# Performance work log

Hardware: AMD Instinct MI355X
Metric: run time of the kernel (lower is better)

## Reference

```python
import jax, jax.numpy as jnp
import numpy as np

LN_EPS = 1e-5


def setup_inputs() -> dict:
    key = jax.random.key(0)
    ks = jax.random.split(key, 5)
    dim, hidden = 512, 8
    B, S = 128, 1024
    x = jax.random.normal(ks[0], (B, S, dim), dtype=jnp.float32)
    # torch Linear: weight [out, in], bias [out]
    w1 = jax.random.normal(ks[1], (hidden, dim), dtype=jnp.float32) * (1.0 / np.sqrt(dim))
    b1 = jax.random.normal(ks[2], (hidden,), dtype=jnp.float32) * 0.02
    w2 = jax.random.normal(ks[3], (dim, hidden), dtype=jnp.float32) * (1.0 / np.sqrt(hidden))
    b2 = jax.random.normal(ks[4], (dim,), dtype=jnp.float32) * 0.02
    gamma = jnp.ones((dim,), dtype=jnp.float32)
    beta = jnp.zeros((dim,), dtype=jnp.float32)
    return {"x": x, "w1": w1, "b1": b1, "w2": w2, "b2": b2,
            "gamma": gamma, "beta": beta}


def _layernorm(y, gamma, beta):
    mu = jnp.mean(y, axis=-1, keepdims=True)
    var = jnp.mean(jnp.square(y - mu), axis=-1, keepdims=True)
    return (y - mu) * jax.lax.rsqrt(var + LN_EPS) * gamma + beta


def reference(x, w1, b1, w2, b2, gamma, beta):
    # y = gelu(gelu(LN(x) @ W1^T + b1) @ W2^T + b2) + x  (exact erf GELU, as torch nn.GELU default)
    y = _layernorm(x, gamma, beta)                       # [B,S,D]
    h = jnp.einsum('bsd,hd->bsh', y, w1) + b1            # [B,S,8]
    h = jax.nn.gelu(h, approximate=False)
    o = jnp.einsum('bsh,dh->bsd', h, w2) + b2            # [B,S,D]
    o = jax.nn.gelu(o, approximate=False)
    return o + x
```

## Files before the change

### kernel.cpp

```cpp
#include <hip/hip_runtime.h>
#include <math.h>

#define DIM 512
#define HID 8
#define LN_EPS 1e-5f

typedef float  f32x4 __attribute__((ext_vector_type(4)));
typedef __fp16 h16x2 __attribute__((ext_vector_type(2)));

#define DPP_XOR1 0xB1
#define DPP_XOR2 0x4E
#define DPP_HM   0x141
#define DPP_ROR8 0x128
#define DPP_ROR4 0x124

template <int CTRL>
__device__ __forceinline__ float dpp_movf(float v) {
    int r = __builtin_amdgcn_update_dpp(0, __builtin_bit_cast(int, v),
                                        CTRL, 0xF, 0xF, true);
    return __builtin_bit_cast(float, r);
}
template <int CTRL>
__device__ __forceinline__ float dpp_addf(float v) {
    return v + dpp_movf<CTRL>(v);
}
__device__ __forceinline__ float readlanef(float v, int lane) {
    return __builtin_bit_cast(float,
        __builtin_amdgcn_readlane(__builtin_bit_cast(int, v), lane));
}

__device__ __forceinline__ float gelu_fast(float v) {
    const float C = 0.044715f;
    const float K = 2.30258819f;
    float v2 = v * v;
    float t  = v * fmaf(C, v2, 1.0f);
    float e  = __builtin_amdgcn_exp2f(K * t);
    float r  = __builtin_amdgcn_rcpf(e + 1.0f);
    return fmaf(-v, r, v);
}

__device__ __forceinline__ float wave_sum(float v) {
    v = dpp_addf<DPP_XOR1>(v);
    v = dpp_addf<DPP_XOR2>(v);
    v = dpp_addf<DPP_HM>(v);
    v = dpp_addf<DPP_ROR8>(v);
    return (readlanef(v, 0) + readlanef(v, 16))
         + (readlanef(v, 32) + readlanef(v, 48));
}

__device__ __forceinline__ float reduce8(float ph[8], int lj) {
#pragma unroll
    for (int j = 0; j < 8; ++j) ph[j] = dpp_addf<DPP_XOR1>(ph[j]);
#pragma unroll
    for (int j = 0; j < 8; ++j) ph[j] = dpp_addf<DPP_XOR2>(ph[j]);
#pragma unroll
    for (int j = 0; j < 8; ++j) ph[j] = dpp_addf<DPP_HM>(ph[j]);
    float sel = ph[0];
    sel = (lj == 1) ? ph[1] : sel;
    sel = (lj == 2) ? ph[2] : sel;
    sel = (lj == 3) ? ph[3] : sel;
    sel = (lj == 4) ? ph[4] : sel;
    sel = (lj == 5) ? ph[5] : sel;
    sel = (lj == 6) ? ph[6] : sel;
    sel = (lj == 7) ? ph[7] : sel;
    sel = dpp_addf<DPP_ROR8>(sel);
    sel += __shfl_xor(sel, 16, 64);
    sel += __shfl_xor(sel, 32, 64);
    return sel;
}

__device__ __forceinline__ void load8(float* dst, const float* __restrict__ src) {
    const f32x4* p = reinterpret_cast<const f32x4*>(src);
    f32x4 a = p[0];
    f32x4 b = p[1];
    dst[0] = a.x; dst[1] = a.y; dst[2] = a.z; dst[3] = a.w;
    dst[4] = b.x; dst[5] = b.y; dst[6] = b.z; dst[7] = b.w;
}

__global__ __launch_bounds__(256)
__attribute__((amdgpu_waves_per_eu(4)))
void mlp_fused_kernel(const float* __restrict__ x,
                      const float* __restrict__ w1,
                      const float* __restrict__ b1,
                      const float* __restrict__ w2,
                      const float* __restrict__ b2,
                      const float* __restrict__ gamma,
                      const float* __restrict__ beta,
                      float* __restrict__ out,
                      int nrows, int rows_per_wave) {
    const int lane  = threadIdx.x & 63;
    const int wav   = threadIdx.x >> 6;
    const int wgid  = blockIdx.x * 4 + wav;
    const int dbase = lane * 8;
    const int lj    = lane & 7;

    const int r0 = wgid * rows_per_wave;
    if (r0 >= nrows) return;
    int r1 = r0 + rows_per_wave;
    if (r1 > nrows) r1 = nrows;

    float gm[8], bt[8];
    load8(gm, gamma + dbase);
    load8(bt, beta  + dbase);

    h16x2 w1p[32];
    float w1sp[8], c1p[8];
#pragma unroll
    for (int j = 0; j < 8; ++j) { w1sp[j] = 0.f; c1p[j] = 0.f; }
#pragma unroll
    for (int j = 0; j < 8; ++j) {
        float raw[8];
        load8(raw, w1 + j * DIM + dbase);
#pragma unroll
        for (int k = 0; k < 8; ++k)
            c1p[j] = fmaf(bt[k], raw[k], c1p[j]);
#pragma unroll
        for (int i = 0; i < 4; ++i) {
            float a = raw[2 * i]     * gm[2 * i];
            float b = raw[2 * i + 1] * gm[2 * i + 1];
            h16x2 p = __builtin_amdgcn_cvt_pkrtz(a, b);
            w1p[j * 4 + i] = p;
            w1sp[j] += (float)p.x + (float)p.y;
        }
    }
    const float W1s = reduce8(w1sp, lj);
    const float b1e = b1[lj] + reduce8(c1p, lj);

    h16x2 w2pk[32];
#pragma unroll
    for (int k = 0; k < 8; ++k)
#pragma unroll
        for (int i = 0; i < 4; ++i) {
            float a = w2[(size_t)(dbase + k) * HID + (lj ^ (2 * i))];
            float b = w2[(size_t)(dbase + k) * HID + (lj ^ (2 * i + 1))];
            w2pk[k * 4 + i] = __builtin_amdgcn_cvt_pkrtz(a, b);
        }

    float b2r[8];
    load8(b2r, b2 + dbase);

    float xv[8];
    load8(xv, x + (size_t)r0 * DIM + dbase);

    for (int r = r0; r < r1; ++r) {
        float xn[8];
        const int rn = (r + 1 < r1) ? (r + 1) : r;
        load8(xn, x + (size_t)rn * DIM + dbase);

        float s = 0.f, q = 0.f;
#pragma unroll
        for (int k = 0; k < 8; ++k) { s += xv[k]; q = fmaf(xv[k], xv[k], q); }

        h16x2 xh[4];
#pragma unroll
        for (int i = 0; i < 4; ++i)
            xh[i] = __builtin_amdgcn_cvt_pkrtz(xv[2 * i], xv[2 * i + 1]);

        float ph[8];
#pragma unroll
        for (int j = 0; j < 8; ++j) {
            float a = 0.f;
#pragma unroll
            for (int i = 0; i < 4; ++i)
                a = __builtin_amdgcn_fdot2(xh[i], w1p[j * 4 + i], a, false);
            ph[j] = a;
        }

        const float sw = wave_sum(s);
        const float qw = wave_sum(q);
        const float Hw = reduce8(ph, lj);

        const float mu  = sw * (1.0f / DIM);
        const float var = qw * (1.0f / DIM) - mu * mu;
        const float rs  = rsqrtf(var + LN_EPS);

        const float h = gelu_fast(fmaf(rs, fmaf(-mu, W1s, Hw), b1e));

        float hj0 = h;
        float hj1 = dpp_movf<DPP_XOR1>(hj0);
        float hj2 = dpp_movf<DPP_XOR2>(hj0);
        float hj3 = dpp_movf<DPP_XOR2>(hj1);
        float hj4 = dpp_movf<DPP_ROR4>(hj0);
        float hj5 = dpp_movf<DPP_ROR4>(hj1);
        float hj6 = dpp_movf<DPP_ROR4>(hj2);
        float hj7 = dpp_movf<DPP_ROR4>(hj3);
        h16x2 hp[4];
        hp[0] = __builtin_amdgcn_cvt_pkrtz(hj0, hj1);
        hp[1] = __builtin_amdgcn_cvt_pkrtz(hj2, hj3);
        hp[2] = __builtin_amdgcn_cvt_pkrtz(hj4, hj5);
        hp[3] = __builtin_amdgcn_cvt_pkrtz(hj6, hj7);

        f32x4 o0, o1;
#pragma unroll
        for (int k = 0; k < 8; ++k) {
            float o = b2r[k];
#pragma unroll
            for (int i = 0; i < 4; ++i)
                o = __builtin_amdgcn_fdot2(hp[i], w2pk[k * 4 + i], o, false);
            float val = gelu_fast(o) + xv[k];
            if (k < 4) o0[k] = val; else o1[k - 4] = val;
        }

        float* po = out + (size_t)r * DIM + dbase;
        __builtin_nontemporal_store(o0, reinterpret_cast<f32x4*>(po));
        __builtin_nontemporal_store(o1, reinterpret_cast<f32x4*>(po) + 1);

#pragma unroll
        for (int k = 0; k < 8; ++k) xv[k] = xn[k];
    }
}

extern "C" void kernel_launch(void* const* d_in, const int* in_sizes, int n_in,
                              void* d_out, int out_size, void* d_ws, size_t ws_size,
                              hipStream_t stream) {
    const float* x     = (const float*)d_in[0];
    const float* w1    = (const float*)d_in[1];
    const float* b1    = (const float*)d_in[2];
    const float* w2    = (const float*)d_in[3];
    const float* b2    = (const float*)d_in[4];
    const float* gamma = (const float*)d_in[5];
    const float* beta  = (const float*)d_in[6];
    float* out = (float*)d_out;

    const int nrows  = in_sizes[0] / DIM;
    const int blocks = 1024;
    const int total_waves = blocks * 4;
    const int rows_per_wave = (nrows + total_waves - 1) / total_waves;

    mlp_fused_kernel<<<blocks, 256, 0, stream>>>(
        x, w1, b1, w2, b2, gamma, beta, out, nrows, rows_per_wave);
}
```

Measured before the change: 143.6 us.

## Stage packed fp16 weights in LDS and double the grid to raise occupancy

Each workgroup now converts W1 (pre-scaled by gamma) and W2 to packed fp16 once into shared memory, with an XOR swizzle on W2, instead of every lane holding 64 packed weight registers. The per-row matvecs read weight vectors back from LDS. The layer-1 activations are broadcast with readlane rather than a DPP permutation. The waves_per_eu hint is dropped and the grid goes from 1024 to 2048 blocks. The aim is lower VGPR pressure and more resident waves to better hide HBM latency on this bandwidth-bound kernel, at the cost of extra LDS reads on every row and a per-block weight setup.

Measured after the change: 168.4 us. +17.2%, slower.

```diff
diff --git a/kernel.cpp b/kernel.cpp
--- a/kernel.cpp
+++ b/kernel.cpp
@@ -7,12 +7,12 @@
 
 typedef float  f32x4 __attribute__((ext_vector_type(4)));
 typedef __fp16 h16x2 __attribute__((ext_vector_type(2)));
+typedef __fp16 h16x8 __attribute__((ext_vector_type(8)));
 
 #define DPP_XOR1 0xB1
 #define DPP_XOR2 0x4E
 #define DPP_HM   0x141
 #define DPP_ROR8 0x128
-#define DPP_ROR4 0x124
 
 template <int CTRL>
 __device__ __forceinline__ float dpp_movf(float v) {
@@ -78,7 +78,6 @@
 }
 
 __global__ __launch_bounds__(256)
-__attribute__((amdgpu_waves_per_eu(4)))
 void mlp_fused_kernel(const float* __restrict__ x,
                       const float* __restrict__ w1,
                       const float* __restrict__ b1,
@@ -88,57 +87,91 @@
                       const float* __restrict__ beta,
                       float* __restrict__ out,
                       int nrows, int rows_per_wave) {
-    const int lane  = threadIdx.x & 63;
-    const int wav   = threadIdx.x >> 6;
-    const int wgid  = blockIdx.x * 4 + wav;
+    __shared__ __fp16 w1h[8 * DIM];
+    __shared__ __fp16 w2h[DIM * HID];
+
+    const int tid  = threadIdx.x;
+    const int lane = tid & 63;
+    const int wav  = tid >> 6;
+    const int lj   = lane & 7;
     const int dbase = lane * 8;
-    const int lj    = lane & 7;
-
+
+    {
+        const int j  = tid >> 5;
+        const int d0 = (tid & 31) * 16;
+        const float* wsrc = w1 + j * DIM + d0;
+        const float* gsrc = gamma + d0;
+        h16x8 p0, p1;
+#pragma unroll
+        for (int i = 0; i < 4; ++i) {
+            float a = wsrc[2 * i]     * gsrc[2 * i];
+            float b = wsrc[2 * i + 1] * gsrc[2 * i + 1];
+            h16x2 p = __builtin_amdgcn_cvt_pkrtz(a, b);
+            p0[2 * i] = p.x; p0[2 * i + 1] = p.y;
+        }
+#pragma unroll
+        for (int i = 0; i < 4; ++i) {
+            float a = wsrc[8 + 2 * i]     * gsrc[8 + 2 * i];
+            float b = wsrc[8 + 2 * i + 1] * gsrc[8 + 2 * i + 1];
+            h16x2 p = __builtin_amdgcn_cvt_pkrtz(a, b);
+            p1[2 * i] = p.x; p1[2 * i + 1] = p.y;
+        }
+        *reinterpret_cast<h16x8*>(&w1h[j * DIM + d0])     = p0;
+        *reinterpret_cast<h16x8*>(&w1h[j * DIM + d0 + 8]) = p1;
+
+#pragma unroll
+        for (int rr = 0; rr < 2; ++rr) {
+            const int d = tid + rr * 256;
+            const float* src = w2 + (size_t)d * HID;
+            f32x4 a = *reinterpret_cast<const f32x4*>(src);
+            f32x4 b = *reinterpret_cast<const f32x4*>(src + 4);
+            h16x8 pk;
+            h16x2 q0 = __builtin_amdgcn_cvt_pkrtz(a.x, a.y);
+            h16x2 q1 = __builtin_amdgcn_cvt_pkrtz(a.z, a.w);
+            h16x2 q2 = __builtin_amdgcn_cvt_pkrtz(b.x, b.y);
+            h16x2 q3 = __builtin_amdgcn_cvt_pkrtz(b.z, b.w);
+            pk[0] = q0.x; pk[1] = q0.y; pk[2] = q1.x; pk[3] = q1.y;
+            pk[4] = q2.x; pk[5] = q2.y; pk[6] = q3.x; pk[7] = q3.y;
+            const int u = ((d >> 3) << 3) + ((d & 7) ^ ((d >> 3) & 7));
+            *reinterpret_cast<h16x8*>(&w2h[u * 8]) = pk;
+        }
+    }
+    __syncthreads();
+
+    float w1sp[8];
+#pragma unroll
+    for (int j = 0; j < 8; ++j) {
+        h16x8 wv = *reinterpret_cast<const h16x8*>(&w1h[j * DIM + dbase]);
+        float a = 0.f;
+#pragma unroll
+        for (int i = 0; i < 8; ++i) a += (float)wv[i];
+        w1sp[j] = a;
+    }
+    const float W1s = reduce8(w1sp, lj);
+
+    float bt[8];
+    load8(bt, beta + dbase);
+    float c1p[8];
+#pragma unroll
+    for (int j = 0; j < 8; ++j) {
+        float raw[8];
+        load8(raw, w1 + j * DIM + dbase);
+        float a = 0.f;
+#pragma unroll
+        for (int k = 0; k < 8; ++k) a = fmaf(bt[k], raw[k], a);
+        c1p[j] = a;
+    }
+    const float b1e = b1[lj] + reduce8(c1p, lj);
+
+    float b2r[8];
+    load8(b2r, b2 + dbase);
+
+    const int wgid = blockIdx.x * 4 + wav;
     const int r0 = wgid * rows_per_wave;
     if (r0 >= nrows) return;
     int r1 = r0 + rows_per_wave;
     if (r1 > nrows) r1 = nrows;
 
-    float gm[8], bt[8];
-    load8(gm, gamma + dbase);
-    load8(bt, beta  + dbase);
-
-    h16x2 w1p[32];
-    float w1sp[8], c1p[8];
-#pragma unroll
-    for (int j = 0; j < 8; ++j) { w1sp[j] = 0.f; c1p[j] = 0.f; }
-#pragma unroll
-    for (int j = 0; j < 8; ++j) {
-        float raw[8];
-        load8(raw, w1 + j * DIM + dbase);
-#pragma unroll
-        for (int k = 0; k < 8; ++k)
-            c1p[j] = fmaf(bt[k], raw[k], c1p[j]);
-#pragma unroll
-        for (int i = 0; i < 4; ++i) {
-            float a = raw[2 * i]     * gm[2 * i];
-            float b = raw[2 * i + 1] * gm[2 * i + 1];
-            h16x2 p = __builtin_amdgcn_cvt_pkrtz(a, b);
-            w1p[j * 4 + i] = p;
-            w1sp[j] += (float)p.x + (float)p.y;
-        }
-    }
-    const float W1s = reduce8(w1sp, lj);
-    const float b1e = b1[lj] + reduce8(c1p, lj);
-
-    h16x2 w2pk[32];
-#pragma unroll
-    for (int k = 0; k < 8; ++k)
-#pragma unroll
-        for (int i = 0; i < 4; ++i) {
-            float a = w2[(size_t)(dbase + k) * HID + (lj ^ (2 * i))];
-            float b = w2[(size_t)(dbase + k) * HID + (lj ^ (2 * i + 1))];
-            w2pk[k * 4 + i] = __builtin_amdgcn_cvt_pkrtz(a, b);
-        }
-
-    float b2r[8];
-    load8(b2r, b2 + dbase);
-
     float xv[8];
     load8(xv, x + (size_t)r0 * DIM + dbase);
 
@@ -159,10 +192,13 @@
         float ph[8];
 #pragma unroll
         for (int j = 0; j < 8; ++j) {
+            h16x8 wv = *reinterpret_cast<const h16x8*>(&w1h[j * DIM + dbase]);
             float a = 0.f;
 #pragma unroll
-            for (int i = 0; i < 4; ++i)
-                a = __builtin_amdgcn_fdot2(xh[i], w1p[j * 4 + i], a, false);
+            for (int i = 0; i < 4; ++i) {
+                h16x2 wp; wp.x = wv[2 * i]; wp.y = wv[2 * i + 1];
+                a = __builtin_amdgcn_fdot2(xh[i], wp, a, false);
+            }
             ph[j] = a;
         }
 
@@ -174,31 +210,29 @@
         const float var = qw * (1.0f / DIM) - mu * mu;
         const float rs  = rsqrtf(var + LN_EPS);
 
-        const float h = gelu_fast(fmaf(rs, fmaf(-mu, W1s, Hw), b1e));
-
-        float hj0 = h;
-        float hj1 = dpp_movf<DPP_XOR1>(hj0);
-        float hj2 = dpp_movf<DPP_XOR2>(hj0);
-        float hj3 = dpp_movf<DPP_XOR2>(hj1);
-        float hj4 = dpp_movf<DPP_ROR4>(hj0);
-        float hj5 = dpp_movf<DPP_ROR4>(hj1);
-        float hj6 = dpp_movf<DPP_ROR4>(hj2);
-        float hj7 = dpp_movf<DPP_ROR4>(hj3);
+        const float hact = gelu_fast(fmaf(rs, fmaf(-mu, W1s, Hw), b1e));
+
+        float hv[8];
+#pragma unroll
+        for (int j = 0; j < 8; ++j) hv[j] = readlanef(hact, j);
         h16x2 hp[4];
-        hp[0] = __builtin_amdgcn_cvt_pkrtz(hj0, hj1);
-        hp[1] = __builtin_amdgcn_cvt_pkrtz(hj2, hj3);
-        hp[2] = __builtin_amdgcn_cvt_pkrtz(hj4, hj5);
-        hp[3] = __builtin_amdgcn_cvt_pkrtz(hj6, hj7);
+#pragma unroll
+        for (int i = 0; i < 4; ++i)
+            hp[i] = __builtin_amdgcn_cvt_pkrtz(hv[2 * i], hv[2 * i + 1]);
 
         f32x4 o0, o1;
 #pragma unroll
-        for (int k = 0; k < 8; ++k) {
-            float o = b2r[k];
-#pragma unroll
-            for (int i = 0; i < 4; ++i)
-                o = __builtin_amdgcn_fdot2(hp[i], w2pk[k * 4 + i], o, false);
-            float val = gelu_fast(o) + xv[k];
-            if (k < 4) o0[k] = val; else o1[k - 4] = val;
+        for (int t = 0; t < 8; ++t) {
+            h16x8 wv = *reinterpret_cast<const h16x8*>(
+                &w2h[(lane * 8 + ((t ^ lj))) * 8]);
+            float o = b2r[t];
+#pragma unroll
+            for (int i = 0; i < 4; ++i) {
+                h16x2 wp; wp.x = wv[2 * i]; wp.y = wv[2 * i + 1];
+                o = __builtin_amdgcn_fdot2(hp[i], wp, o, false);
+            }
+            float val = gelu_fast(o) + xv[t];
+            if (t < 4) o0[t] = val; else o1[t - 4] = val;
         }
 
         float* po = out + (size_t)r * DIM + dbase;
@@ -223,7 +257,7 @@
     float* out = (float*)d_out;
 
     const int nrows  = in_sizes[0] / DIM;
-    const int blocks = 1024;
+    const int blocks = 2048;
     const int total_waves = blocks * 4;
     const int rows_per_wave = (nrows + total_waves - 1) / total_waves;
 
```
